# Kernel tuning notes

Measured on AMD Instinct MI355X. Metric: run time of the kernel, lower is better.

Reference implementation:

```python
import jax, jax.numpy as jnp
import numpy as np

B, S, D = 4, 2048, 128

def _phi(x, W, d):
    # original: phi(x) = (1/sqrt(M)) * exp(-0.5*||x||_2) * exp(W @ x), M = d
    proj = jnp.exp(jnp.einsum('...d,md->...m', x, W))          # [..., d]
    scale = jnp.exp(-0.5 * jnp.linalg.norm(x, axis=-1, keepdims=True))
    return (scale / jnp.sqrt(jnp.asarray(d, x.dtype))) * proj

def setup_inputs() -> dict:
    key = jax.random.key(0)
    k1, k2, k3, k4 = jax.random.split(key, 4)
    # scale 0.1 keeps exp(W @ x) well within fp32 range
    K = jax.random.normal(k1, (B, S, D), dtype=jnp.float32) * 0.1
    Q = jax.random.normal(k2, (B, S, D), dtype=jnp.float32) * 0.1
    V = jax.random.normal(k3, (B, S, D), dtype=jnp.float32) * 0.1
    W_phi = jax.random.normal(k4, (D, D), dtype=jnp.float32)
    sent_embed_slice = jnp.zeros((B, 1), dtype=jnp.float32)
    return {"K": K, "Q": Q, "V": V, "sent_embed_slice": sent_embed_slice,
            "max_seq_length": S, "qkv_size": D, "W_phi": W_phi}

def reference(K, Q, V, sent_embed_slice, max_seq_length, qkv_size, W_phi):
    d = qkv_size
    phiK = _phi(K, W_phi, d)   # [B, S, d]
    phiQ = _phi(Q, W_phi, d)   # [B, S, d]
    Bn = K.shape[0]

    def step(carry, inp):
        Mst, Nst = carry                       # [B, d, d], [B, d]
        pk, v, pq = inp                        # each [B, d]
        Mst = Mst + pk[:, :, None] * v[:, None, :]   # cumulative outer product
        Nst = Nst + pk                               # cumulative feature sum
        num = jnp.einsum('bd,bde->be', pq, Mst)      # phi(q) @ M
        r = jnp.einsum('bd,bd->b', pq, Nst)          # phi(q) . N
        out = num / (r + jnp.sign(r) * 1e-6)[:, None]
        return (Mst, Nst), out

    init = (jnp.zeros((Bn, d, d), K.dtype), jnp.zeros((Bn, d), K.dtype))
    xs = (jnp.swapaxes(phiK, 0, 1), jnp.swapaxes(V, 0, 1), jnp.swapaxes(phiQ, 0, 1))
    _, outs = jax.lax.scan(step, init, xs)    # outs: [S, B, d]
    return jnp.swapaxes(outs, 0, 1)           # [B, S, d]
```

## Files before the change

### kernel.cpp

```cpp
#include <hip/hip_runtime.h>

typedef float v4 __attribute__((ext_vector_type(4)));
typedef short s8v __attribute__((ext_vector_type(8)));
typedef float f4v __attribute__((ext_vector_type(4)));
typedef unsigned short u16;
typedef u16 us2 __attribute__((ext_vector_type(2)));
typedef u16 us4 __attribute__((ext_vector_type(4)));
typedef u16 us8 __attribute__((ext_vector_type(8)));

#define OFF_PHIKB 0
#define OFF_PHIQB 524288
#define OFF_KVTB  1048576
#define OFF_N32   2097152

__device__ inline u16 f2bf(float f) {
  union { float f; unsigned u; } v; v.f = f;
  unsigned r = v.u + 0x7fffu + ((v.u >> 16) & 1u);
  return (u16)(r >> 16);
}
__device__ inline float bf2f(u16 h) {
  union { unsigned u; float f; } v; v.u = ((unsigned)h) << 16; return v.f;
}

__global__ __launch_bounds__(512) void phikv_kernel(
    const float* __restrict__ K, const float* __restrict__ Q,
    const float* __restrict__ V, const float* __restrict__ W,
    u16* __restrict__ phiKb, u16* __restrict__ phiQb,
    u16* __restrict__ KVTb, float* __restrict__ N32) {
  __shared__ __align__(16) u16 smem[27136];
  __shared__ float srowsq[64];
  __shared__ float scl[64];
  u16* Xb = smem;
  u16* Wb = smem + 8704;
  u16* Pb = smem;
  u16* KdT = smem + 8704;
  u16* Vt = smem + 17920;

  const int tid = threadIdx.x;
  const bool isK = (blockIdx.y == 0);
  const float* X = isK ? K : Q;
  u16* outPhi = isK ? phiKb : phiQb;
  const int row0 = blockIdx.x * 64;
  const int wv = tid >> 6;
  const int lane = tid & 63;
  const int q = lane >> 4;
  const int ln = lane & 15;

  v4 vpa[2], vpb[2];
  if (isK) {
#pragma unroll
    for (int k = 0; k < 2; k++) {
      int j = tid + k * 512;
      int s0 = (j & 31) * 2;
      int e4 = (j >> 5) * 4;
      vpa[k] = *(const v4*)&V[(size_t)(row0 + s0) * 128 + e4];
      vpb[k] = *(const v4*)&V[(size_t)(row0 + s0 + 1) * 128 + e4];
    }
  }

#pragma unroll
  for (int k = 0; k < 4; k++) {
    int j = tid + k * 512;
    int r = j >> 5;
    int c4 = (j & 31) * 4;
    v4 x = *(const v4*)&X[(size_t)(row0 + r) * 128 + c4];
    us4 xb;
    float p = 0.f;
#pragma unroll
    for (int i = 0; i < 4; i++) { xb[i] = f2bf(x[i]); p += x[i] * x[i]; }
    *(us4*)&Xb[r * 136 + c4] = xb;
    p += __shfl_down(p, 16, 32);
    p += __shfl_down(p, 8, 32);
    p += __shfl_down(p, 4, 32);
    p += __shfl_down(p, 2, 32);
    p += __shfl_down(p, 1, 32);
    if ((tid & 31) == 0) srowsq[r] = p;
  }
#pragma unroll
  for (int k = 0; k < 8; k++) {
    int j = tid + k * 512;
    int r = j >> 5;
    int c4 = (j & 31) * 4;
    v4 w = *(const v4*)&W[(size_t)r * 128 + c4];
    us4 wb;
#pragma unroll
    for (int i = 0; i < 4; i++) wb[i] = f2bf(w[i]);
    *(us4*)&Wb[r * 136 + c4] = wb;
  }
  __syncthreads();
  if (tid < 64)
    scl[tid] = 0.08838834764831845f * __expf(-0.5f * sqrtf(srowsq[tid]));

  const int tr = wv >> 1;
  const int cb = (wv & 1) * 4;
  f4v acc[4];
#pragma unroll
  for (int i = 0; i < 4; i++) acc[i] = (f4v){0.f, 0.f, 0.f, 0.f};
#pragma unroll
  for (int ks = 0; ks < 4; ks++) {
    s8v a = *(const s8v*)&Xb[(tr * 16 + ln) * 136 + ks * 32 + q * 8];
#pragma unroll
    for (int i = 0; i < 4; i++) {
      s8v bb = *(const s8v*)&Wb[((cb + i) * 16 + ln) * 136 + ks * 32 + q * 8];
      acc[i] = __builtin_amdgcn_mfma_f32_16x16x32_bf16(a, bb, acc[i], 0, 0, 0);
    }
  }
  __syncthreads();

#pragma unroll
  for (int i = 0; i < 4; i++) {
    const int ct = cb + i;
    us4 col;
#pragma unroll
    for (int r = 0; r < 4; r++) {
      int row = tr * 16 + q * 4 + r;
      u16 hv = f2bf(scl[row] * __expf(acc[i][r]));
      Pb[row * 136 + ct * 16 + ln] = hv;
      col[r] = hv;
    }
    if (isK) *(us4*)&KdT[(ct * 16 + ln) * 72 + tr * 16 + q * 4] = col;
  }
  if (isK) {
#pragma unroll
    for (int k = 0; k < 2; k++) {
      int j = tid + k * 512;
      int s0 = (j & 31) * 2;
      int e4 = (j >> 5) * 4;
#pragma unroll
      for (int i = 0; i < 4; i++) {
        us2 w2 = {f2bf(vpa[k][i]), f2bf(vpb[k][i])};
        *(us2*)&Vt[(e4 + i) * 72 + s0] = w2;
      }
    }
  }
  __syncthreads();

#pragma unroll
  for (int k = 0; k < 2; k++) {
    int j = tid + k * 512;
    int r = j >> 4;
    int d8 = (j & 15) * 8;
    *(us8*)&outPhi[(size_t)(row0 + r) * 128 + d8] = *(const us8*)&Pb[r * 136 + d8];
  }
  if (!isK) return;

  const int b = row0 >> 11;
  const int c = (row0 >> 6) & 31;

  if (tid < 128) {
    float ns = 0.f;
#pragma unroll
    for (int s = 0; s < 64; s++) ns += bf2f(KdT[tid * 72 + s]);
    N32[(size_t)(b * 32 + c) * 128 + tid] = ns;
  }

  {
    const int et = wv;
    s8v a0 = *(const s8v*)&Vt[(et * 16 + ln) * 72 + q * 8];
    s8v a1 = *(const s8v*)&Vt[(et * 16 + ln) * 72 + 32 + q * 8];
    f4v ac[8];
#pragma unroll
    for (int dt = 0; dt < 8; dt++) ac[dt] = (f4v){0.f, 0.f, 0.f, 0.f};
#pragma unroll
    for (int dt = 0; dt < 8; dt++) {
      s8v b0 = *(const s8v*)&KdT[(dt * 16 + ln) * 72 + q * 8];
      ac[dt] = __builtin_amdgcn_mfma_f32_16x16x32_bf16(a0, b0, ac[dt], 0, 0, 0);
      s8v b1 = *(const s8v*)&KdT[(dt * 16 + ln) * 72 + 32 + q * 8];
      ac[dt] = __builtin_amdgcn_mfma_f32_16x16x32_bf16(a1, b1, ac[dt], 0, 0, 0);
    }
#pragma unroll
    for (int dt = 0; dt < 8; dt++)
#pragma unroll
      for (int r = 0; r < 4; r++) {
        int e = et * 16 + q * 4 + r;
        int d = dt * 16 + ln;
        KVTb[((size_t)(b * 128 + e) * 32 + c) * 128 + d] = f2bf(ac[dt][r]);
      }
  }
}

__global__ __launch_bounds__(256) void out_kernel(
    const u16* __restrict__ phiKb, const u16* __restrict__ phiQb,
    const float* __restrict__ V, const u16* __restrict__ KVTb,
    const float* __restrict__ N32, float* __restrict__ out) {
  __shared__ __align__(16) u16 Qs[64 * 136];
  __shared__ __align__(16) u16 Ks[64 * 136];
  __shared__ __align__(16) u16 Ms[32 * 136];
  __shared__ __align__(16) u16 Vt[32 * 72];
  __shared__ __align__(16) u16 Ps[64 * 72];
  __shared__ float Ns[128];
  __shared__ float rs[64];

  const int tid = threadIdx.x;
  const int id = blockIdx.x;
  const int h = id & 3;
  const int c = 31 - ((id >> 2) & 31);
  const int b = id >> 7;
  const int srow0 = b * 2048 + c * 64;
  const int ecol0 = h * 32;
  const int wv = tid >> 6;
  const int lane = tid & 63;
  const int q = lane >> 4;
  const int ln = lane & 15;

  const int vs0 = (tid & 31) * 2;
  const int ve4 = (tid >> 5) * 4;
  v4 va = *(const v4*)&V[(size_t)(srow0 + vs0) * 128 + ecol0 + ve4];
  v4 vb = *(const v4*)&V[(size_t)(srow0 + vs0 + 1) * 128 + ecol0 + ve4];

#pragma unroll
  for (int k = 0; k < 4; k++) {
    int j = tid + k * 256;
    int t = j >> 4;
    int d8 = (j & 15) * 8;
    *(us8*)&Qs[t * 136 + d8] = *(const us8*)&phiQb[(size_t)(srow0 + t) * 128 + d8];
    *(us8*)&Ks[t * 136 + d8] = *(const us8*)&phiKb[(size_t)(srow0 + t) * 128 + d8];
  }

  {
    const int se = tid >> 4;
    const int sd8 = (tid & 15) * 8;
    const u16* src0 =
        &KVTb[((size_t)(b * 128 + ecol0 + se) * 32) * 128 + sd8];
    const u16* src1 =
        &KVTb[((size_t)(b * 128 + ecol0 + 16 + se) * 32) * 128 + sd8];
    float m0[8], m1[8];
#pragma unroll
    for (int i = 0; i < 8; i++) { m0[i] = 0.f; m1[i] = 0.f; }
    for (int cp = 0; cp < c; cp++) {
      us8 k0 = *(const us8*)&src0[cp * 128];
      us8 k1 = *(const us8*)&src1[cp * 128];
#pragma unroll
      for (int i = 0; i < 8; i++) {
        m0[i] += bf2f(k0[i]);
        m1[i] += bf2f(k1[i]);
      }
    }
    us8 w0, w1;
#pragma unroll
    for (int i = 0; i < 8; i++) { w0[i] = f2bf(m0[i]); w1[i] = f2bf(m1[i]); }
    *(us8*)&Ms[se * 136 + sd8] = w0;
    *(us8*)&Ms[(16 + se) * 136 + sd8] = w1;
  }
  if (tid < 128) {
    float na = 0.f;
    for (int cp = 0; cp < c; cp++)
      na += N32[(size_t)(b * 32 + cp) * 128 + tid];
    Ns[tid] = na;
  }
#pragma unroll
  for (int i = 0; i < 4; i++) {
    us2 w2 = {f2bf(va[i]), f2bf(vb[i])};
    *(us2*)&Vt[(ve4 + i) * 72 + vs0] = w2;
  }
  __syncthreads();

  {
    const int tr = wv;
    for (int tc = 0; tc < 4; tc++) {
      f4v acc = {0.f, 0.f, 0.f, 0.f};
      if (tc <= tr) {
#pragma unroll
        for (int ks = 0; ks < 4; ks++) {
          s8v a = *(const s8v*)&Qs[(tr * 16 + ln) * 136 + ks * 32 + q * 8];
          s8v bb = *(const s8v*)&Ks[(tc * 16 + ln) * 136 + ks * 32 + q * 8];
          acc = __builtin_amdgcn_mfma_f32_16x16x32_bf16(a, bb, acc, 0, 0, 0);
        }
      }
      const int s_g = tc * 16 + ln;
#pragma unroll
      for (int r = 0; r < 4; r++) {
        int t_g = tr * 16 + q * 4 + r;
        Ps[t_g * 72 + s_g] = f2bf(s_g <= t_g ? acc[r] : 0.f);
      }
    }
  }
  __syncthreads();

  {
    const int t = tid >> 2;
    const int p4 = tid & 3;
    float rsl = 0.f;
#pragma unroll
    for (int s = p4; s < 64; s += 4) rsl += bf2f(Ps[t * 72 + s]);
#pragma unroll
    for (int d = p4; d < 128; d += 4) rsl += bf2f(Qs[t * 136 + d]) * Ns[d];
    rsl += __shfl_down(rsl, 2, 4);
    rsl += __shfl_down(rsl, 1, 4);
    if (p4 == 0) rs[t] = rsl;
  }

  const int et = wv & 1;
  f4v acc2[2];
#pragma unroll
  for (int i = 0; i < 2; i++) acc2[i] = (f4v){0.f, 0.f, 0.f, 0.f};
#pragma unroll
  for (int i = 0; i < 2; i++) {
    const int tr2 = (wv >> 1) + 2 * i;
#pragma unroll
    for (int ks2 = 0; ks2 < 2; ks2++) {
      s8v a_p = *(const s8v*)&Ps[(tr2 * 16 + ln) * 72 + ks2 * 32 + q * 8];
      s8v b_v = *(const s8v*)&Vt[(et * 16 + ln) * 72 + ks2 * 32 + q * 8];
      acc2[i] = __builtin_amdgcn_mfma_f32_16x16x32_bf16(a_p, b_v, acc2[i], 0, 0, 0);
    }
#pragma unroll
    for (int ks = 0; ks < 4; ks++) {
      s8v a_q = *(const s8v*)&Qs[(tr2 * 16 + ln) * 136 + ks * 32 + q * 8];
      s8v b_m = *(const s8v*)&Ms[(et * 16 + ln) * 136 + ks * 32 + q * 8];
      acc2[i] = __builtin_amdgcn_mfma_f32_16x16x32_bf16(a_q, b_m, acc2[i], 0, 0, 0);
    }
  }
  __syncthreads();

#pragma unroll
  for (int i = 0; i < 2; i++) {
    const int tr2 = (wv >> 1) + 2 * i;
#pragma unroll
    for (int r = 0; r < 4; r++) {
      int t_g = tr2 * 16 + q * 4 + r;
      float rv = rs[t_g];
      float den = rv + (rv > 0.f ? 1e-6f : (rv < 0.f ? -1e-6f : 0.f));
      out[(size_t)(srow0 + t_g) * 128 + ecol0 + et * 16 + ln] =
          acc2[i][r] / den;
    }
  }
}

extern "C" void kernel_launch(void* const* d_in, const int* in_sizes, int n_in,
                              void* d_out, int out_size, void* d_ws,
                              size_t ws_size, hipStream_t stream) {
  (void)in_sizes; (void)n_in; (void)out_size; (void)ws_size;
  const float* K = (const float*)d_in[0];
  const float* Q = (const float*)d_in[1];
  const float* V = (const float*)d_in[2];
  const float* W = (const float*)d_in[6];
  float* out = (float*)d_out;
  float* ws = (float*)d_ws;

  u16* phiKb = (u16*)(ws + OFF_PHIKB);
  u16* phiQb = (u16*)(ws + OFF_PHIQB);
  u16* KVTb = (u16*)(ws + OFF_KVTB);
  float* N32 = ws + OFF_N32;

  phikv_kernel<<<dim3(128, 2), 512, 0, stream>>>(K, Q, V, W, phiKb, phiQb,
                                                 KVTb, N32);
  out_kernel<<<512, 256, 0, stream>>>(phiKb, phiQb, V, KVTb, N32, out);
}
```

Measured before the change: 103.8 us.

## Split out_kernel into 16-column slices and read phiK straight from global

Launches twice as many out_kernel blocks, each owning 16 output columns instead of 32, so the prefix-sum of KV chunks per block is halved and there is more parallelism. It drops the Ks shared tile and loads phiK MFMA operands directly from global memory. It batches the prefix-sum loads eight chunks at a time, changes block ordering to chunk-major, and sets a launch-bounds occupancy hint. The cost is that the QK^T and row-sum work is duplicated across twice as many blocks.

```diff
diff --git a/kernel.cpp b/kernel.cpp
--- a/kernel.cpp
+++ b/kernel.cpp
@@ -1,6 +1,7 @@
 #include <hip/hip_runtime.h>
 
 typedef float v4 __attribute__((ext_vector_type(4)));
+typedef float v2 __attribute__((ext_vector_type(2)));
 typedef short s8v __attribute__((ext_vector_type(8)));
 typedef float f4v __attribute__((ext_vector_type(4)));
 typedef unsigned short u16;
@@ -179,34 +180,34 @@
   }
 }
 
-__global__ __launch_bounds__(256) void out_kernel(
+__global__ __launch_bounds__(256, 4) void out_kernel(
     const u16* __restrict__ phiKb, const u16* __restrict__ phiQb,
     const float* __restrict__ V, const u16* __restrict__ KVTb,
     const float* __restrict__ N32, float* __restrict__ out) {
   __shared__ __align__(16) u16 Qs[64 * 136];
-  __shared__ __align__(16) u16 Ks[64 * 136];
-  __shared__ __align__(16) u16 Ms[32 * 136];
-  __shared__ __align__(16) u16 Vt[32 * 72];
+  __shared__ __align__(16) u16 Ms[16 * 136];
+  __shared__ __align__(16) u16 Vt[16 * 72];
   __shared__ __align__(16) u16 Ps[64 * 72];
   __shared__ float Ns[128];
   __shared__ float rs[64];
 
   const int tid = threadIdx.x;
   const int id = blockIdx.x;
-  const int h = id & 3;
-  const int c = 31 - ((id >> 2) & 31);
-  const int b = id >> 7;
+  const int c = id >> 5;
+  const int g = id & 31;
+  const int b = g >> 3;
+  const int h8 = g & 7;
   const int srow0 = b * 2048 + c * 64;
-  const int ecol0 = h * 32;
+  const int ecol0 = h8 * 16;
   const int wv = tid >> 6;
   const int lane = tid & 63;
   const int q = lane >> 4;
   const int ln = lane & 15;
 
   const int vs0 = (tid & 31) * 2;
-  const int ve4 = (tid >> 5) * 4;
-  v4 va = *(const v4*)&V[(size_t)(srow0 + vs0) * 128 + ecol0 + ve4];
-  v4 vb = *(const v4*)&V[(size_t)(srow0 + vs0 + 1) * 128 + ecol0 + ve4];
+  const int ve2 = (tid >> 5) * 2;
+  v2 va = *(const v2*)&V[(size_t)(srow0 + vs0) * 128 + ecol0 + ve2];
+  v2 vb = *(const v2*)&V[(size_t)(srow0 + vs0 + 1) * 128 + ecol0 + ve2];
 
 #pragma unroll
   for (int k = 0; k < 4; k++) {
@@ -214,56 +215,64 @@
     int t = j >> 4;
     int d8 = (j & 15) * 8;
     *(us8*)&Qs[t * 136 + d8] = *(const us8*)&phiQb[(size_t)(srow0 + t) * 128 + d8];
-    *(us8*)&Ks[t * 136 + d8] = *(const us8*)&phiKb[(size_t)(srow0 + t) * 128 + d8];
   }
 
   {
     const int se = tid >> 4;
     const int sd8 = (tid & 15) * 8;
-    const u16* src0 =
+    const u16* src =
         &KVTb[((size_t)(b * 128 + ecol0 + se) * 32) * 128 + sd8];
-    const u16* src1 =
-        &KVTb[((size_t)(b * 128 + ecol0 + 16 + se) * 32) * 128 + sd8];
-    float m0[8], m1[8];
-#pragma unroll
-    for (int i = 0; i < 8; i++) { m0[i] = 0.f; m1[i] = 0.f; }
-    for (int cp = 0; cp < c; cp++) {
-      us8 k0 = *(const us8*)&src0[cp * 128];
-      us8 k1 = *(const us8*)&src1[cp * 128];
-#pragma unroll
-      for (int i = 0; i < 8; i++) {
-        m0[i] += bf2f(k0[i]);
-        m1[i] += bf2f(k1[i]);
-      }
-    }
-    us8 w0, w1;
-#pragma unroll
-    for (int i = 0; i < 8; i++) { w0[i] = f2bf(m0[i]); w1[i] = f2bf(m1[i]); }
-    *(us8*)&Ms[se * 136 + sd8] = w0;
-    *(us8*)&Ms[(16 + se) * 136 + sd8] = w1;
+    float m[8];
+#pragma unroll
+    for (int i = 0; i < 8; i++) m[i] = 0.f;
+    for (int base = 0; base < c; base += 8) {
+      us8 t8[8];
+#pragma unroll
+      for (int u = 0; u < 8; u++)
+        if (base + u < c) t8[u] = *(const us8*)&src[(base + u) * 128];
+#pragma unroll
+      for (int u = 0; u < 8; u++)
+        if (base + u < c)
+#pragma unroll
+          for (int i = 0; i < 8; i++) m[i] += bf2f(t8[u][i]);
+    }
+    us8 w8;
+#pragma unroll
+    for (int i = 0; i < 8; i++) w8[i] = f2bf(m[i]);
+    *(us8*)&Ms[se * 136 + sd8] = w8;
   }
   if (tid < 128) {
     float na = 0.f;
-    for (int cp = 0; cp < c; cp++)
-      na += N32[(size_t)(b * 32 + cp) * 128 + tid];
+    for (int base = 0; base < c; base += 8) {
+      float t[8];
+#pragma unroll
+      for (int u = 0; u < 8; u++)
+        t[u] = (base + u < c) ? N32[(size_t)(b * 32 + base + u) * 128 + tid]
+                              : 0.f;
+#pragma unroll
+      for (int u = 0; u < 8; u++) na += t[u];
+    }
     Ns[tid] = na;
   }
-#pragma unroll
-  for (int i = 0; i < 4; i++) {
-    us2 w2 = {f2bf(va[i]), f2bf(vb[i])};
-    *(us2*)&Vt[(ve4 + i) * 72 + vs0] = w2;
+  {
+    us2 w0 = {f2bf(va[0]), f2bf(vb[0])};
+    us2 w1 = {f2bf(va[1]), f2bf(vb[1])};
+    *(us2*)&Vt[ve2 * 72 + vs0] = w0;
+    *(us2*)&Vt[(ve2 + 1) * 72 + vs0] = w1;
   }
   __syncthreads();
 
   {
     const int tr = wv;
+    const u16* kbase = &phiKb[(size_t)srow0 * 128];
     for (int tc = 0; tc < 4; tc++) {
       f4v acc = {0.f, 0.f, 0.f, 0.f};
       if (tc <= tr) {
 #pragma unroll
         for (int ks = 0; ks < 4; ks++) {
           s8v a = *(const s8v*)&Qs[(tr * 16 + ln) * 136 + ks * 32 + q * 8];
-          s8v bb = *(const s8v*)&Ks[(tc * 16 + ln) * 136 + ks * 32 + q * 8];
+          s8v bb =
+              *(const s8v*)&kbase[(size_t)(tc * 16 + ln) * 128 + ks * 32 + q * 8];
           acc = __builtin_amdgcn_mfma_f32_16x16x32_bf16(a, bb, acc, 0, 0, 0);
         }
       }
@@ -290,38 +299,32 @@
     if (p4 == 0) rs[t] = rsl;
   }
 
-  const int et = wv & 1;
-  f4v acc2[2];
-#pragma unroll
-  for (int i = 0; i < 2; i++) acc2[i] = (f4v){0.f, 0.f, 0.f, 0.f};
-#pragma unroll
-  for (int i = 0; i < 2; i++) {
-    const int tr2 = (wv >> 1) + 2 * i;
+  f4v acc2 = {0.f, 0.f, 0.f, 0.f};
+  {
+    const int tr2 = wv;
 #pragma unroll
     for (int ks2 = 0; ks2 < 2; ks2++) {
       s8v a_p = *(const s8v*)&Ps[(tr2 * 16 + ln) * 72 + ks2 * 32 + q * 8];
-      s8v b_v = *(const s8v*)&Vt[(et * 16 + ln) * 72 + ks2 * 32 + q * 8];
-      acc2[i] = __builtin_amdgcn_mfma_f32_16x16x32_bf16(a_p, b_v, acc2[i], 0, 0, 0);
+      s8v b_v = *(const s8v*)&Vt[ln * 72 + ks2 * 32 + q * 8];
+      acc2 = __builtin_amdgcn_mfma_f32_16x16x32_bf16(a_p, b_v, acc2, 0, 0, 0);
     }
 #pragma unroll
     for (int ks = 0; ks < 4; ks++) {
       s8v a_q = *(const s8v*)&Qs[(tr2 * 16 + ln) * 136 + ks * 32 + q * 8];
-      s8v b_m = *(const s8v*)&Ms[(et * 16 + ln) * 136 + ks * 32 + q * 8];
-      acc2[i] = __builtin_amdgcn_mfma_f32_16x16x32_bf16(a_q, b_m, acc2[i], 0, 0, 0);
-    }
-  }
-  __syncthreads();
-
-#pragma unroll
-  for (int i = 0; i < 2; i++) {
-    const int tr2 = (wv >> 1) + 2 * i;
+      s8v b_m = *(const s8v*)&Ms[ln * 136 + ks * 32 + q * 8];
+      acc2 = __builtin_amdgcn_mfma_f32_16x16x32_bf16(a_q, b_m, acc2, 0, 0, 0);
+    }
+  }
+  __syncthreads();
+
+  {
+    const int tr2 = wv;
 #pragma unroll
     for (int r = 0; r < 4; r++) {
       int t_g = tr2 * 16 + q * 4 + r;
       float rv = rs[t_g];
       float den = rv + (rv > 0.f ? 1e-6f : (rv < 0.f ? -1e-6f : 0.f));
-      out[(size_t)(srow0 + t_g) * 128 + ecol0 + et * 16 + ln] =
-          acc2[i][r] / den;
+      out[(size_t)(srow0 + t_g) * 128 + ecol0 + ln] = acc2[r] / den;
     }
   }
 }
@@ -344,5 +347,5 @@
 
   phikv_kernel<<<dim3(128, 2), 512, 0, stream>>>(K, Q, V, W, phiKb, phiQb,
                                                  KVTb, N32);
-  out_kernel<<<512, 256, 0, stream>>>(phiKb, phiQb, V, KVTb, N32, out);
-}
+  out_kernel<<<1024, 256, 0, stream>>>(phiKb, phiQb, V, KVTb, N32, out);
+}
```

After: 95.44 us. 8.0% less time.
